# Kernel tuning notes

Hardware: AMD Instinct MI355X
Metric: run time of the kernel (lower is better)

Reference implementation:

```python
import jax, jax.numpy as jnp
import numpy as np

T, E, H, V, B, MAX_NB = 12, 8192, 256, 800, 256, 8
M = T * E  # total messages; slot 0 of the buffer is the zero pad


def setup_inputs() -> dict:
    key = jax.random.key(0)
    ks = jax.random.split(key, 16)
    s = 1.0 / np.sqrt(H)

    x_ids = jax.random.randint(ks[0], (T, E), 0, V)
    # neighbor message indices: at depth t only messages from earlier depths
    # (slots 1..t*E) or the zero pad (slot 0) are valid, matching BFS order.
    rows = []
    for t in range(T):
        kt = jax.random.fold_in(ks[1], t)
        rows.append(jax.random.randint(kt, (E, MAX_NB), 0, max(1, t * E + 1)))
    nei_idx = jnp.stack(rows)
    root_wid = jax.random.randint(ks[2], (B,), 0, V)
    root_nei = jax.random.randint(ks[3], (B, MAX_NB), 0, M + 1)

    f32 = jnp.float32
    return {
        "x_ids": x_ids, "nei_idx": nei_idx,
        "root_wid": root_wid, "root_nei": root_nei,
        "embedding": jax.random.normal(ks[4], (V, H), f32) * s,
        "Wz": jax.random.normal(ks[5], (2 * H, H), f32) * s,
        "bz": jnp.zeros((H,), f32),
        "Wr": jax.random.normal(ks[6], (H, H), f32) * s,
        "Ur": jax.random.normal(ks[7], (H, H), f32) * s,
        "bur": jnp.zeros((H,), f32),
        "Wh": jax.random.normal(ks[8], (2 * H, H), f32) * s,
        "bh": jnp.zeros((H,), f32),
        "Wo": jax.random.normal(ks[9], (2 * H, H), f32) * s,
        "bo": jnp.zeros((H,), f32),
    }


def _gru(x, h_nei, Wz, bz, Wr, Ur, bur, Wh, bh):
    # x: [E,H], h_nei: [E,MAX_NB,H] -- JT-VAE tree GRU
    sum_h = h_nei.sum(axis=1)
    z = jax.nn.sigmoid(jnp.concatenate([x, sum_h], axis=-1) @ Wz + bz)
    r1 = (x @ Wr)[:, None, :]                 # [E,1,H]
    r2 = h_nei @ Ur + bur                     # [E,MAX_NB,H]
    r = jax.nn.sigmoid(r1 + r2)
    sum_gated = (r * h_nei).sum(axis=1)
    pre_h = jnp.tanh(jnp.concatenate([x, sum_gated], axis=-1) @ Wh + bh)
    return (1.0 - z) * sum_h + z * pre_h


def reference(x_ids, nei_idx, root_wid, root_nei, embedding,
              Wz, bz, Wr, Ur, bur, Wh, bh, Wo, bo):
    h0 = jnp.zeros((1 + M, H), embedding.dtype)  # slot 0 == padding

    def step(h, inp):
        t, xid, nidx = inp
        x = embedding[xid]          # [E,H] gather
        h_nei = h[nidx]             # [E,MAX_NB,H] gather
        new_h = _gru(x, h_nei, Wz, bz, Wr, Ur, bur, Wh, bh)
        h = jax.lax.dynamic_update_slice(h, new_h, (1 + t * E, 0))
        return h, None

    h, _ = jax.lax.scan(step, h0, (jnp.arange(T), x_ids, nei_idx))

    # node_aggregate on roots
    x_root = embedding[root_wid]               # [B,H]
    sum_nei = h[root_nei].sum(axis=1)          # [B,H]
    root_vecs = jax.nn.relu(jnp.concatenate([x_root, sum_nei], axis=-1) @ Wo + bo)
    return h, root_vecs
```

## Files before the change

kernel.cpp:

```cpp
#include <hip/hip_runtime.h>
#include <hip/hip_bf16.h>
#include <math.h>

#define T_ 12
#define E_ 8192
#define H_ 256
#define V_ 800
#define B_ 256
#define NB_ 8
#define M_ (T_*E_)
#define TM 16
#define HP (H_ + 8)

typedef __attribute__((ext_vector_type(8))) short bf16x8;
typedef __attribute__((ext_vector_type(4))) float f32x4;

#define LOG2E_ 1.44269504088896f

__device__ __forceinline__ float fexp2_(float x) { return __builtin_amdgcn_exp2f(x); }
__device__ __forceinline__ float frcp_(float x)  { return __builtin_amdgcn_rcpf(x); }
__device__ __forceinline__ float fsig(float x) {
    return frcp_(1.0f + fexp2_(-LOG2E_ * x));
}
__device__ __forceinline__ float ftanh(float x) {
    return 1.0f - 2.0f * frcp_(fexp2_(2.0f * LOG2E_ * x) + 1.0f);
}

__device__ __forceinline__ short f2bf(float x) {
    unsigned u = __float_as_uint(x);
    unsigned r = (u + 0x7fffu + ((u >> 16) & 1u)) >> 16;
    return (short)r;
}
__device__ __forceinline__ float bf2f(unsigned short s) {
    return __uint_as_float(((unsigned)s) << 16);
}
__device__ __forceinline__ float hu_h(unsigned v) { return __uint_as_float(v << 16); }
__device__ __forceinline__ float hu_u(unsigned v) { return __uint_as_float(v & 0xffff0000u); }
__device__ __forceinline__ unsigned pack2(float a, float b) {
    return (unsigned)(unsigned short)f2bf(a) | ((unsigned)(unsigned short)f2bf(b) << 16);
}

__global__ __launch_bounds__(256) void k_wconv(
    const float* __restrict__ Wz, const float* __restrict__ Wh, const float* __restrict__ Ur,
    short* __restrict__ Wzt, short* __restrict__ Wht, short* __restrict__ Urt,
    float* __restrict__ h, unsigned* __restrict__ hu)
{
    if (blockIdx.x == 768) {
        h[threadIdx.x] = 0.0f;
        hu[threadIdx.x] = 0u;
        return;
    }
    int tid = blockIdx.x * 256 + threadIdx.x;
    int w = tid >> 16;
    int idx = tid & 65535;
    int n = idx >> 8, k = idx & 255;
    if (w == 0)      Wzt[idx] = f2bf(Wz[(size_t)(256 + k) * H_ + n]);
    else if (w == 1) Wht[idx] = f2bf(Wh[(size_t)(256 + k) * H_ + n]);
    else             Urt[idx] = f2bf(Ur[(size_t)k * H_ + n]);
}

__global__ __launch_bounds__(256) void gemm_pre(
    const float* __restrict__ emb,
    const float* __restrict__ Wr, const float* __restrict__ Wz,
    const float* __restrict__ Wh, const float* __restrict__ Wo,
    const float* __restrict__ bur, const float* __restrict__ bz,
    const float* __restrict__ bh, const float* __restrict__ bo,
    float* __restrict__ eWr, float* __restrict__ eWz,
    float* __restrict__ eWh, float* __restrict__ eWo)
{
    const float* Bm; const float* bias; float* C;
    switch (blockIdx.z) {
        case 0: Bm = Wr; bias = bur; C = eWr; break;
        case 1: Bm = Wz; bias = bz;  C = eWz; break;
        case 2: Bm = Wh; bias = bh;  C = eWh; break;
        default: Bm = Wo; bias = bo; C = eWo; break;
    }
    __shared__ float As[16][64];
    __shared__ float Bs[16][64];
    const int tid = threadIdx.x;
    const int bm = blockIdx.x * 64;
    const int bn = blockIdx.y * 64;
    const int a_m = tid & 63;
    const int a_k = (tid >> 6) << 2;
    const int b_k = tid >> 4;
    const int b_n = (tid & 15) << 2;
    const int tx = tid & 15, ty = tid >> 4;

    float acc[4][4] = {};
    const bool a_ok = (bm + a_m) < V_;
    const float* Ap = emb + (size_t)(bm + a_m) * H_ + a_k;
    const float* Bp = Bm + (size_t)b_k * H_ + bn + b_n;

    for (int k0 = 0; k0 < H_; k0 += 16) {
        float4 av = a_ok ? *(const float4*)(Ap + k0) : make_float4(0.f, 0.f, 0.f, 0.f);
        float4 bv = *(const float4*)(Bp + (size_t)k0 * H_);
        __syncthreads();
        As[a_k + 0][a_m] = av.x;
        As[a_k + 1][a_m] = av.y;
        As[a_k + 2][a_m] = av.z;
        As[a_k + 3][a_m] = av.w;
        *(float4*)&Bs[b_k][b_n] = bv;
        __syncthreads();
#pragma unroll
        for (int k = 0; k < 16; ++k) {
            const float4 a4 = *(const float4*)&As[k][ty << 2];
            const float4 b4 = *(const float4*)&Bs[k][tx << 2];
            const float ar[4] = {a4.x, a4.y, a4.z, a4.w};
            const float br[4] = {b4.x, b4.y, b4.z, b4.w};
#pragma unroll
            for (int i = 0; i < 4; ++i)
#pragma unroll
                for (int j = 0; j < 4; ++j)
                    acc[i][j] = fmaf(ar[i], br[j], acc[i][j]);
        }
    }

    const int col = bn + (tx << 2);
#pragma unroll
    for (int i = 0; i < 4; ++i) {
        const int row = bm + (ty << 2) + i;
        if (row >= V_) break;
        *(float4*)(C + (size_t)row * H_ + col) =
            make_float4(acc[i][0] + bias[col], acc[i][1] + bias[col + 1],
                        acc[i][2] + bias[col + 2], acc[i][3] + bias[col + 3]);
    }
}

__global__ __launch_bounds__(256) void k_pack(
    const float* __restrict__ eWz, const float* __restrict__ eWh,
    unsigned* __restrict__ eWzh)
{
    const int i = blockIdx.x * 256 + threadIdx.x;
    eWzh[i] = pack2(eWz[i], eWh[i]);
}

__global__ __launch_bounds__(512, 4) void k_step(
    int t,
    const int* __restrict__ x_ids, const int* __restrict__ nei_idx,
    float* __restrict__ h, unsigned* __restrict__ hu,
    const float* __restrict__ eWr, const unsigned* __restrict__ eWzh,
    const short* __restrict__ Wzt, const short* __restrict__ Wht,
    const short* __restrict__ Urt,
    int do_ur)
{
    __shared__ int   idx[TM][NB_];
    __shared__ int   xw[TM];
    __shared__ short shB[TM][HP];
    __shared__ short sgB[TM][HP];
    __shared__ short hB[TM][HP];

    const int tid = threadIdx.x;
    const int e0 = blockIdx.x * TM;

    if (tid < TM * NB_) {
        int r = tid >> 3, j = tid & 7;
        idx[r][j] = nei_idx[((size_t)t * E_ + e0 + r) * NB_ + j];
    }
    if (tid < TM) xw[tid] = x_ids[t * E_ + e0 + tid];
    __syncthreads();

    {
        const int c0 = (tid & 63) * 4;
        const int ra = (tid >> 6) * 2;
        const int rb = ra + 1;
        if (t == 0) {
            *(uint2*)&shB[ra][c0] = make_uint2(0u, 0u);
            *(uint2*)&sgB[ra][c0] = make_uint2(0u, 0u);
            *(uint2*)&shB[rb][c0] = make_uint2(0u, 0u);
            *(uint2*)&sgB[rb][c0] = make_uint2(0u, 0u);
        } else {
            uint4 va[NB_], vb[NB_];
#pragma unroll
            for (int j = 0; j < NB_; ++j)
                va[j] = *(const uint4*)(hu + (size_t)idx[ra][j] * H_ + c0);
#pragma unroll
            for (int j = 0; j < NB_; ++j)
                vb[j] = *(const uint4*)(hu + (size_t)idx[rb][j] * H_ + c0);
            const float4 r1a = *(const float4*)(eWr + (size_t)xw[ra] * H_ + c0);
            const float4 r1b = *(const float4*)(eWr + (size_t)xw[rb] * H_ + c0);

            float sa0 = 0.f, sa1 = 0.f, sa2 = 0.f, sa3 = 0.f;
            float ga0 = 0.f, ga1 = 0.f, ga2 = 0.f, ga3 = 0.f;
#pragma unroll
            for (int j = 0; j < NB_; ++j) {
                const float h0 = hu_h(va[j].x); sa0 += h0;
                ga0 = fmaf(fsig(r1a.x + hu_u(va[j].x)), h0, ga0);
                const float h1 = hu_h(va[j].y); sa1 += h1;
                ga1 = fmaf(fsig(r1a.y + hu_u(va[j].y)), h1, ga1);
                const float h2 = hu_h(va[j].z); sa2 += h2;
                ga2 = fmaf(fsig(r1a.z + hu_u(va[j].z)), h2, ga2);
                const float h3 = hu_h(va[j].w); sa3 += h3;
                ga3 = fmaf(fsig(r1a.w + hu_u(va[j].w)), h3, ga3);
            }
            *(uint2*)&shB[ra][c0] = make_uint2(pack2(sa0, sa1), pack2(sa2, sa3));
            *(uint2*)&sgB[ra][c0] = make_uint2(pack2(ga0, ga1), pack2(ga2, ga3));

            float sb0 = 0.f, sb1 = 0.f, sb2 = 0.f, sb3 = 0.f;
            float gb0 = 0.f, gb1 = 0.f, gb2 = 0.f, gb3 = 0.f;
#pragma unroll
            for (int j = 0; j < NB_; ++j) {
                const float h0 = hu_h(vb[j].x); sb0 += h0;
                gb0 = fmaf(fsig(r1b.x + hu_u(vb[j].x)), h0, gb0);
                const float h1 = hu_h(vb[j].y); sb1 += h1;
                gb1 = fmaf(fsig(r1b.y + hu_u(vb[j].y)), h1, gb1);
                const float h2 = hu_h(vb[j].z); sb2 += h2;
                gb2 = fmaf(fsig(r1b.z + hu_u(vb[j].z)), h2, gb2);
                const float h3 = hu_h(vb[j].w); sb3 += h3;
                gb3 = fmaf(fsig(r1b.w + hu_u(vb[j].w)), h3, gb3);
            }
            *(uint2*)&shB[rb][c0] = make_uint2(pack2(sb0, sb1), pack2(sb2, sb3));
            *(uint2*)&sgB[rb][c0] = make_uint2(pack2(gb0, gb1), pack2(gb2, gb3));
        }
    }
    __syncthreads();

    const int lane = tid & 63;
    const int wave = tid >> 6;
    const int n0 = wave * 32;
    const int quad = lane >> 4, c = lane & 15;
    const int kq = quad * 8;

    f32x4 accZ[2], accH[2];
#pragma unroll
    for (int i = 0; i < 2; ++i) { accZ[i] = (f32x4)(0.0f); accH[i] = (f32x4)(0.0f); }

#pragma unroll
    for (int k0 = 0; k0 < H_; k0 += 32) {
        const bf16x8 a1 = *(const bf16x8*)&shB[c][k0 + kq];
        const bf16x8 a2 = *(const bf16x8*)&sgB[c][k0 + kq];
#pragma unroll
        for (int ni = 0; ni < 2; ++ni) {
            const size_t boff = (size_t)(n0 + ni * 16 + c) * H_ + k0 + kq;
            const bf16x8 b1 = *(const bf16x8*)(Wzt + boff);
            const bf16x8 b2 = *(const bf16x8*)(Wht + boff);
            accZ[ni] = __builtin_amdgcn_mfma_f32_16x16x32_bf16(a1, b1, accZ[ni], 0, 0, 0);
            accH[ni] = __builtin_amdgcn_mfma_f32_16x16x32_bf16(a2, b2, accH[ni], 0, 0, 0);
        }
    }

    float* h_t = h + (size_t)(1 + t * E_) * H_;
#pragma unroll
    for (int reg = 0; reg < 4; ++reg) {
        const int r = quad * 4 + reg;
        const int xr = xw[r];
#pragma unroll
        for (int ni = 0; ni < 2; ++ni) {
            const int col = n0 + ni * 16 + c;
            const unsigned zh = eWzh[(size_t)xr * H_ + col];
            const float z   = fsig(accZ[ni][reg] + hu_h(zh));
            const float pre = ftanh(accH[ni][reg] + hu_u(zh));
            const float hv = (1.0f - z) * bf2f((unsigned short)shB[r][col]) + z * pre;
            h_t[(size_t)(e0 + r) * H_ + col] = hv;
            hB[r][col] = f2bf(hv);
        }
    }

    if (!do_ur) return;
    __syncthreads();

    {
        f32x4 accU[2];
        accU[0] = (f32x4)(0.0f); accU[1] = (f32x4)(0.0f);
#pragma unroll
        for (int k0 = 0; k0 < H_; k0 += 32) {
            const bf16x8 a = *(const bf16x8*)&hB[c][k0 + kq];
#pragma unroll
            for (int ni = 0; ni < 2; ++ni) {
                const bf16x8 b = *(const bf16x8*)(Urt + (size_t)(n0 + ni * 16 + c) * H_ + k0 + kq);
                accU[ni] = __builtin_amdgcn_mfma_f32_16x16x32_bf16(a, b, accU[ni], 0, 0, 0);
            }
        }
        unsigned* hu_t = hu + (size_t)(1 + t * E_) * H_;
#pragma unroll
        for (int reg = 0; reg < 4; ++reg) {
            const int r = quad * 4 + reg;
#pragma unroll
            for (int ni = 0; ni < 2; ++ni) {
                const int col = n0 + ni * 16 + c;
                const unsigned ubits = (unsigned)(unsigned short)f2bf(accU[ni][reg]);
                const unsigned hbits = (unsigned)(unsigned short)hB[r][col];
                hu_t[(size_t)(e0 + r) * H_ + col] = (ubits << 16) | hbits;
            }
        }
    }
}

__global__ __launch_bounds__(256) void k_root(
    const int* __restrict__ root_wid, const int* __restrict__ root_nei,
    const float* __restrict__ h, const float* __restrict__ eWo,
    const float* __restrict__ Wo, float* __restrict__ out)
{
    const int b = blockIdx.x, d = threadIdx.x;
    __shared__ float sn[H_];
    __shared__ int idx[NB_];
    if (d < NB_) idx[d] = root_nei[b * NB_ + d];
    __syncthreads();
    float s = 0.0f;
#pragma unroll
    for (int j = 0; j < NB_; ++j) s += h[(size_t)idx[j] * H_ + d];
    sn[d] = s;
    __syncthreads();
    float acc = eWo[(size_t)root_wid[b] * H_ + d];
    for (int k = 0; k < H_; ++k)
        acc = fmaf(sn[k], Wo[(size_t)(H_ + k) * H_ + d], acc);
    out[(size_t)b * H_ + d] = fmaxf(acc, 0.0f);
}

extern "C" void kernel_launch(void* const* d_in, const int* in_sizes, int n_in,
                              void* d_out, int out_size, void* d_ws, size_t ws_size,
                              hipStream_t stream)
{
    const int*   x_ids    = (const int*)d_in[0];
    const int*   nei_idx  = (const int*)d_in[1];
    const int*   root_wid = (const int*)d_in[2];
    const int*   root_nei = (const int*)d_in[3];
    const float* emb      = (const float*)d_in[4];
    const float* Wz       = (const float*)d_in[5];
    const float* bz       = (const float*)d_in[6];
    const float* Wr       = (const float*)d_in[7];
    const float* Ur       = (const float*)d_in[8];
    const float* bur      = (const float*)d_in[9];
    const float* Wh       = (const float*)d_in[10];
    const float* bh       = (const float*)d_in[11];
    const float* Wo       = (const float*)d_in[12];
    const float* bo       = (const float*)d_in[13];

    float* h        = (float*)d_out;
    float* root_out = h + (size_t)(1 + M_) * H_;

    unsigned* hu = (unsigned*)d_ws;
    float* eWr  = (float*)(hu + (size_t)(1 + M_) * H_);
    float* eWz  = eWr  + (size_t)V_ * H_;
    float* eWh  = eWz  + (size_t)V_ * H_;
    float* eWo  = eWh  + (size_t)V_ * H_;
    short* Wzt  = (short*)(eWo + (size_t)V_ * H_);
    short* Wht  = Wzt + 65536;
    short* Urt  = Wht + 65536;
    unsigned* eWzh = (unsigned*)(Urt + 65536);

    k_wconv<<<dim3(769), dim3(256), 0, stream>>>(Wz, Wh, Ur, Wzt, Wht, Urt, h, hu);
    gemm_pre<<<dim3((V_ + 63) / 64, 4, 4), dim3(256), 0, stream>>>(
        emb, Wr, Wz, Wh, Wo, bur, bz, bh, bo, eWr, eWz, eWh, eWo);
    k_pack<<<dim3(V_ * H_ / 256), dim3(256), 0, stream>>>(eWz, eWh, eWzh);

    for (int t = 0; t < T_; ++t) {
        k_step<<<dim3(E_ / TM), dim3(512), 0, stream>>>(
            t, x_ids, nei_idx, h, hu, eWr, eWzh, Wzt, Wht, Urt,
            (t < T_ - 1) ? 1 : 0);
    }

    k_root<<<dim3(B_), dim3(256), 0, stream>>>(root_wid, root_nei, h, eWo, Wo, root_out);
}
```

Measured before the change: 552.3 us.

## Double rows per step block and fuse bf16 packing into precompute GEMM

Raises the step kernel's row tile from 16 to 32 messages per block. Each wave now runs two 16-row MFMA groups that share every Wz/Wh/Ur weight fragment, halving weight reloads per row. Launch bounds drop to 2 blocks per CU to allow more registers and shared memory, at the cost of occupancy and half as many blocks per step. It also writes the packed bf16 z/h embedding products directly from the precompute GEMM and removes the separate pack kernel and its fp32 intermediates.

```diff
diff --git a/kernel.cpp b/kernel.cpp
--- a/kernel.cpp
+++ b/kernel.cpp
@@ -9,7 +9,7 @@
 #define B_ 256
 #define NB_ 8
 #define M_ (T_*E_)
-#define TM 16
+#define TM 32
 #define HP (H_ + 8)
 
 typedef __attribute__((ext_vector_type(8))) short bf16x8;
@@ -65,15 +65,15 @@
     const float* __restrict__ Wh, const float* __restrict__ Wo,
     const float* __restrict__ bur, const float* __restrict__ bz,
     const float* __restrict__ bh, const float* __restrict__ bo,
-    float* __restrict__ eWr, float* __restrict__ eWz,
-    float* __restrict__ eWh, float* __restrict__ eWo)
-{
-    const float* Bm; const float* bias; float* C;
+    float* __restrict__ eWr, unsigned* __restrict__ eWzh,
+    float* __restrict__ eWo)
+{
+    const float* Bm; const float* bias;
     switch (blockIdx.z) {
-        case 0: Bm = Wr; bias = bur; C = eWr; break;
-        case 1: Bm = Wz; bias = bz;  C = eWz; break;
-        case 2: Bm = Wh; bias = bh;  C = eWh; break;
-        default: Bm = Wo; bias = bo; C = eWo; break;
+        case 0: Bm = Wr; bias = bur; break;
+        case 1: Bm = Wz; bias = bz;  break;
+        case 2: Bm = Wh; bias = bh;  break;
+        default: Bm = Wo; bias = bo; break;
     }
     __shared__ float As[16][64];
     __shared__ float Bs[16][64];
@@ -116,25 +116,28 @@
     }
 
     const int col = bn + (tx << 2);
+    const int z = blockIdx.z;
 #pragma unroll
     for (int i = 0; i < 4; ++i) {
         const int row = bm + (ty << 2) + i;
         if (row >= V_) break;
-        *(float4*)(C + (size_t)row * H_ + col) =
-            make_float4(acc[i][0] + bias[col], acc[i][1] + bias[col + 1],
-                        acc[i][2] + bias[col + 2], acc[i][3] + bias[col + 3]);
-    }
-}
-
-__global__ __launch_bounds__(256) void k_pack(
-    const float* __restrict__ eWz, const float* __restrict__ eWh,
-    unsigned* __restrict__ eWzh)
-{
-    const int i = blockIdx.x * 256 + threadIdx.x;
-    eWzh[i] = pack2(eWz[i], eWh[i]);
-}
-
-__global__ __launch_bounds__(512, 4) void k_step(
+        const float v0 = acc[i][0] + bias[col];
+        const float v1 = acc[i][1] + bias[col + 1];
+        const float v2 = acc[i][2] + bias[col + 2];
+        const float v3 = acc[i][3] + bias[col + 3];
+        if (z == 0) {
+            *(float4*)(eWr + (size_t)row * H_ + col) = make_float4(v0, v1, v2, v3);
+        } else if (z == 3) {
+            *(float4*)(eWo + (size_t)row * H_ + col) = make_float4(v0, v1, v2, v3);
+        } else {
+            short* base = (short*)(eWzh + (size_t)row * H_ + col) + (z - 1);
+            base[0] = f2bf(v0); base[2] = f2bf(v1);
+            base[4] = f2bf(v2); base[6] = f2bf(v3);
+        }
+    }
+}
+
+__global__ __launch_bounds__(512, 2) void k_step(
     int t,
     const int* __restrict__ x_ids, const int* __restrict__ nei_idx,
     float* __restrict__ h, unsigned* __restrict__ hu,
@@ -161,55 +164,58 @@
 
     {
         const int c0 = (tid & 63) * 4;
-        const int ra = (tid >> 6) * 2;
-        const int rb = ra + 1;
+        const int rbase = (tid >> 6) * 4;
         if (t == 0) {
-            *(uint2*)&shB[ra][c0] = make_uint2(0u, 0u);
-            *(uint2*)&sgB[ra][c0] = make_uint2(0u, 0u);
-            *(uint2*)&shB[rb][c0] = make_uint2(0u, 0u);
-            *(uint2*)&sgB[rb][c0] = make_uint2(0u, 0u);
+#pragma unroll
+            for (int rr = 0; rr < 4; ++rr) {
+                *(uint2*)&shB[rbase + rr][c0] = make_uint2(0u, 0u);
+                *(uint2*)&sgB[rbase + rr][c0] = make_uint2(0u, 0u);
+            }
         } else {
-            uint4 va[NB_], vb[NB_];
-#pragma unroll
-            for (int j = 0; j < NB_; ++j)
-                va[j] = *(const uint4*)(hu + (size_t)idx[ra][j] * H_ + c0);
-#pragma unroll
-            for (int j = 0; j < NB_; ++j)
-                vb[j] = *(const uint4*)(hu + (size_t)idx[rb][j] * H_ + c0);
-            const float4 r1a = *(const float4*)(eWr + (size_t)xw[ra] * H_ + c0);
-            const float4 r1b = *(const float4*)(eWr + (size_t)xw[rb] * H_ + c0);
-
-            float sa0 = 0.f, sa1 = 0.f, sa2 = 0.f, sa3 = 0.f;
-            float ga0 = 0.f, ga1 = 0.f, ga2 = 0.f, ga3 = 0.f;
-#pragma unroll
-            for (int j = 0; j < NB_; ++j) {
-                const float h0 = hu_h(va[j].x); sa0 += h0;
-                ga0 = fmaf(fsig(r1a.x + hu_u(va[j].x)), h0, ga0);
-                const float h1 = hu_h(va[j].y); sa1 += h1;
-                ga1 = fmaf(fsig(r1a.y + hu_u(va[j].y)), h1, ga1);
-                const float h2 = hu_h(va[j].z); sa2 += h2;
-                ga2 = fmaf(fsig(r1a.z + hu_u(va[j].z)), h2, ga2);
-                const float h3 = hu_h(va[j].w); sa3 += h3;
-                ga3 = fmaf(fsig(r1a.w + hu_u(va[j].w)), h3, ga3);
-            }
-            *(uint2*)&shB[ra][c0] = make_uint2(pack2(sa0, sa1), pack2(sa2, sa3));
-            *(uint2*)&sgB[ra][c0] = make_uint2(pack2(ga0, ga1), pack2(ga2, ga3));
-
-            float sb0 = 0.f, sb1 = 0.f, sb2 = 0.f, sb3 = 0.f;
-            float gb0 = 0.f, gb1 = 0.f, gb2 = 0.f, gb3 = 0.f;
-#pragma unroll
-            for (int j = 0; j < NB_; ++j) {
-                const float h0 = hu_h(vb[j].x); sb0 += h0;
-                gb0 = fmaf(fsig(r1b.x + hu_u(vb[j].x)), h0, gb0);
-                const float h1 = hu_h(vb[j].y); sb1 += h1;
-                gb1 = fmaf(fsig(r1b.y + hu_u(vb[j].y)), h1, gb1);
-                const float h2 = hu_h(vb[j].z); sb2 += h2;
-                gb2 = fmaf(fsig(r1b.z + hu_u(vb[j].z)), h2, gb2);
-                const float h3 = hu_h(vb[j].w); sb3 += h3;
-                gb3 = fmaf(fsig(r1b.w + hu_u(vb[j].w)), h3, gb3);
-            }
-            *(uint2*)&shB[rb][c0] = make_uint2(pack2(sb0, sb1), pack2(sb2, sb3));
-            *(uint2*)&sgB[rb][c0] = make_uint2(pack2(gb0, gb1), pack2(gb2, gb3));
+            for (int rr = 0; rr < 4; rr += 2) {
+                const int ra = rbase + rr, rb = ra + 1;
+                uint4 va[NB_], vb[NB_];
+#pragma unroll
+                for (int j = 0; j < NB_; ++j)
+                    va[j] = *(const uint4*)(hu + (size_t)idx[ra][j] * H_ + c0);
+#pragma unroll
+                for (int j = 0; j < NB_; ++j)
+                    vb[j] = *(const uint4*)(hu + (size_t)idx[rb][j] * H_ + c0);
+                const float4 r1a = *(const float4*)(eWr + (size_t)xw[ra] * H_ + c0);
+                const float4 r1b = *(const float4*)(eWr + (size_t)xw[rb] * H_ + c0);
+
+                float sa0 = 0.f, sa1 = 0.f, sa2 = 0.f, sa3 = 0.f;
+                float ga0 = 0.f, ga1 = 0.f, ga2 = 0.f, ga3 = 0.f;
+#pragma unroll
+                for (int j = 0; j < NB_; ++j) {
+                    const float h0 = hu_h(va[j].x); sa0 += h0;
+                    ga0 = fmaf(fsig(r1a.x + hu_u(va[j].x)), h0, ga0);
+                    const float h1 = hu_h(va[j].y); sa1 += h1;
+                    ga1 = fmaf(fsig(r1a.y + hu_u(va[j].y)), h1, ga1);
+                    const float h2 = hu_h(va[j].z); sa2 += h2;
+                    ga2 = fmaf(fsig(r1a.z + hu_u(va[j].z)), h2, ga2);
+                    const float h3 = hu_h(va[j].w); sa3 += h3;
+                    ga3 = fmaf(fsig(r1a.w + hu_u(va[j].w)), h3, ga3);
+                }
+                *(uint2*)&shB[ra][c0] = make_uint2(pack2(sa0, sa1), pack2(sa2, sa3));
+                *(uint2*)&sgB[ra][c0] = make_uint2(pack2(ga0, ga1), pack2(ga2, ga3));
+
+                float sb0 = 0.f, sb1 = 0.f, sb2 = 0.f, sb3 = 0.f;
+                float gb0 = 0.f, gb1 = 0.f, gb2 = 0.f, gb3 = 0.f;
+#pragma unroll
+                for (int j = 0; j < NB_; ++j) {
+                    const float h0 = hu_h(vb[j].x); sb0 += h0;
+                    gb0 = fmaf(fsig(r1b.x + hu_u(vb[j].x)), h0, gb0);
+                    const float h1 = hu_h(vb[j].y); sb1 += h1;
+                    gb1 = fmaf(fsig(r1b.y + hu_u(vb[j].y)), h1, gb1);
+                    const float h2 = hu_h(vb[j].z); sb2 += h2;
+                    gb2 = fmaf(fsig(r1b.z + hu_u(vb[j].z)), h2, gb2);
+                    const float h3 = hu_h(vb[j].w); sb3 += h3;
+                    gb3 = fmaf(fsig(r1b.w + hu_u(vb[j].w)), h3, gb3);
+                }
+                *(uint2*)&shB[rb][c0] = make_uint2(pack2(sb0, sb1), pack2(sb2, sb3));
+                *(uint2*)&sgB[rb][c0] = make_uint2(pack2(gb0, gb1), pack2(gb2, gb3));
+            }
         }
     }
     __syncthreads();
@@ -220,38 +226,47 @@
     const int quad = lane >> 4, c = lane & 15;
     const int kq = quad * 8;
 
-    f32x4 accZ[2], accH[2];
-#pragma unroll
-    for (int i = 0; i < 2; ++i) { accZ[i] = (f32x4)(0.0f); accH[i] = (f32x4)(0.0f); }
+    f32x4 accZ[2][2], accH[2][2];
+#pragma unroll
+    for (int rg = 0; rg < 2; ++rg)
+#pragma unroll
+        for (int i = 0; i < 2; ++i) { accZ[rg][i] = (f32x4)(0.0f); accH[rg][i] = (f32x4)(0.0f); }
 
 #pragma unroll
     for (int k0 = 0; k0 < H_; k0 += 32) {
-        const bf16x8 a1 = *(const bf16x8*)&shB[c][k0 + kq];
-        const bf16x8 a2 = *(const bf16x8*)&sgB[c][k0 + kq];
+        const bf16x8 a1lo = *(const bf16x8*)&shB[c][k0 + kq];
+        const bf16x8 a2lo = *(const bf16x8*)&sgB[c][k0 + kq];
+        const bf16x8 a1hi = *(const bf16x8*)&shB[16 + c][k0 + kq];
+        const bf16x8 a2hi = *(const bf16x8*)&sgB[16 + c][k0 + kq];
 #pragma unroll
         for (int ni = 0; ni < 2; ++ni) {
             const size_t boff = (size_t)(n0 + ni * 16 + c) * H_ + k0 + kq;
             const bf16x8 b1 = *(const bf16x8*)(Wzt + boff);
             const bf16x8 b2 = *(const bf16x8*)(Wht + boff);
-            accZ[ni] = __builtin_amdgcn_mfma_f32_16x16x32_bf16(a1, b1, accZ[ni], 0, 0, 0);
-            accH[ni] = __builtin_amdgcn_mfma_f32_16x16x32_bf16(a2, b2, accH[ni], 0, 0, 0);
+            accZ[0][ni] = __builtin_amdgcn_mfma_f32_16x16x32_bf16(a1lo, b1, accZ[0][ni], 0, 0, 0);
+            accH[0][ni] = __builtin_amdgcn_mfma_f32_16x16x32_bf16(a2lo, b2, accH[0][ni], 0, 0, 0);
+            accZ[1][ni] = __builtin_amdgcn_mfma_f32_16x16x32_bf16(a1hi, b1, accZ[1][ni], 0, 0, 0);
+            accH[1][ni] = __builtin_amdgcn_mfma_f32_16x16x32_bf16(a2hi, b2, accH[1][ni], 0, 0, 0);
         }
     }
 
     float* h_t = h + (size_t)(1 + t * E_) * H_;
 #pragma unroll
-    for (int reg = 0; reg < 4; ++reg) {
-        const int r = quad * 4 + reg;
-        const int xr = xw[r];
-#pragma unroll
-        for (int ni = 0; ni < 2; ++ni) {
-            const int col = n0 + ni * 16 + c;
-            const unsigned zh = eWzh[(size_t)xr * H_ + col];
-            const float z   = fsig(accZ[ni][reg] + hu_h(zh));
-            const float pre = ftanh(accH[ni][reg] + hu_u(zh));
-            const float hv = (1.0f - z) * bf2f((unsigned short)shB[r][col]) + z * pre;
-            h_t[(size_t)(e0 + r) * H_ + col] = hv;
-            hB[r][col] = f2bf(hv);
+    for (int rg = 0; rg < 2; ++rg) {
+#pragma unroll
+        for (int reg = 0; reg < 4; ++reg) {
+            const int r = rg * 16 + quad * 4 + reg;
+            const int xr = xw[r];
+#pragma unroll
+            for (int ni = 0; ni < 2; ++ni) {
+                const int col = n0 + ni * 16 + c;
+                const unsigned zh = eWzh[(size_t)xr * H_ + col];
+                const float z   = fsig(accZ[rg][ni][reg] + hu_h(zh));
+                const float pre = ftanh(accH[rg][ni][reg] + hu_u(zh));
+                const float hv = (1.0f - z) * bf2f((unsigned short)shB[r][col]) + z * pre;
+                h_t[(size_t)(e0 + r) * H_ + col] = hv;
+                hB[r][col] = f2bf(hv);
+            }
         }
     }
 
@@ -259,27 +274,33 @@
     __syncthreads();
 
     {
-        f32x4 accU[2];
-        accU[0] = (f32x4)(0.0f); accU[1] = (f32x4)(0.0f);
+        f32x4 accU[2][2];
+#pragma unroll
+        for (int rg = 0; rg < 2; ++rg) { accU[rg][0] = (f32x4)(0.0f); accU[rg][1] = (f32x4)(0.0f); }
 #pragma unroll
         for (int k0 = 0; k0 < H_; k0 += 32) {
-            const bf16x8 a = *(const bf16x8*)&hB[c][k0 + kq];
+            const bf16x8 alo = *(const bf16x8*)&hB[c][k0 + kq];
+            const bf16x8 ahi = *(const bf16x8*)&hB[16 + c][k0 + kq];
 #pragma unroll
             for (int ni = 0; ni < 2; ++ni) {
                 const bf16x8 b = *(const bf16x8*)(Urt + (size_t)(n0 + ni * 16 + c) * H_ + k0 + kq);
-                accU[ni] = __builtin_amdgcn_mfma_f32_16x16x32_bf16(a, b, accU[ni], 0, 0, 0);
+                accU[0][ni] = __builtin_amdgcn_mfma_f32_16x16x32_bf16(alo, b, accU[0][ni], 0, 0, 0);
+                accU[1][ni] = __builtin_amdgcn_mfma_f32_16x16x32_bf16(ahi, b, accU[1][ni], 0, 0, 0);
             }
         }
         unsigned* hu_t = hu + (size_t)(1 + t * E_) * H_;
 #pragma unroll
-        for (int reg = 0; reg < 4; ++reg) {
-            const int r = quad * 4 + reg;
-#pragma unroll
-            for (int ni = 0; ni < 2; ++ni) {
-                const int col = n0 + ni * 16 + c;
-                const unsigned ubits = (unsigned)(unsigned short)f2bf(accU[ni][reg]);
-                const unsigned hbits = (unsigned)(unsigned short)hB[r][col];
-                hu_t[(size_t)(e0 + r) * H_ + col] = (ubits << 16) | hbits;
+        for (int rg = 0; rg < 2; ++rg) {
+#pragma unroll
+            for (int reg = 0; reg < 4; ++reg) {
+                const int r = rg * 16 + quad * 4 + reg;
+#pragma unroll
+                for (int ni = 0; ni < 2; ++ni) {
+                    const int col = n0 + ni * 16 + c;
+                    const unsigned ubits = (unsigned)(unsigned short)f2bf(accU[rg][ni][reg]);
+                    const unsigned hbits = (unsigned)(unsigned short)hB[r][col];
+                    hu_t[(size_t)(e0 + r) * H_ + col] = (ubits << 16) | hbits;
+                }
             }
         }
     }
@@ -330,18 +351,15 @@
 
     unsigned* hu = (unsigned*)d_ws;
     float* eWr  = (float*)(hu + (size_t)(1 + M_) * H_);
-    float* eWz  = eWr  + (size_t)V_ * H_;
-    float* eWh  = eWz  + (size_t)V_ * H_;
-    float* eWo  = eWh  + (size_t)V_ * H_;
-    short* Wzt  = (short*)(eWo + (size_t)V_ * H_);
+    float* eWo  = eWr  + (size_t)V_ * H_;
+    unsigned* eWzh = (unsigned*)(eWo + (size_t)V_ * H_);
+    short* Wzt  = (short*)(eWzh + (size_t)V_ * H_);
     short* Wht  = Wzt + 65536;
     short* Urt  = Wht + 65536;
-    unsigned* eWzh = (unsigned*)(Urt + 65536);
 
     k_wconv<<<dim3(769), dim3(256), 0, stream>>>(Wz, Wh, Ur, Wzt, Wht, Urt, h, hu);
     gemm_pre<<<dim3((V_ + 63) / 64, 4, 4), dim3(256), 0, stream>>>(
-        emb, Wr, Wz, Wh, Wo, bur, bz, bh, bo, eWr, eWz, eWh, eWo);
-    k_pack<<<dim3(V_ * H_ / 256), dim3(256), 0, stream>>>(eWz, eWh, eWzh);
+        emb, Wr, Wz, Wh, Wo, bur, bz, bh, bo, eWr, eWzh, eWo);
 
     for (int t = 0; t < T_; ++t) {
         k_step<<<dim3(E_ / TM), dim3(512), 0, stream>>>(
```

New measurement: 451.8 us. -18.2%, faster.
